# Performance work log

Measured on AMD Instinct MI355X. Metric: run time of the kernel, lower is better.

## Reference

```python
import jax, jax.numpy as jnp
import numpy as np

LORA_RANK = 16
LORA_ALPHA = 16
LORA_SCALE = LORA_ALPHA / LORA_RANK


def setup_inputs() -> dict:
    key = jax.random.key(0)
    k1, k2, k3, k4, k5 = jax.random.split(key, 5)
    B, S, D_IN, D_OUT, N_LORA, R = 8, 2048, 4096, 4096, 3, LORA_RANK
    std = 1.0 / np.sqrt(D_IN)
    x = jax.random.normal(k1, (B, S, D_IN), dtype=jnp.float32)
    weight = jax.random.truncated_normal(k2, -3.0, 3.0, (D_OUT, D_IN), dtype=jnp.float32) * std
    bias = jax.random.normal(k3, (D_OUT,), dtype=jnp.float32) * 0.01
    lora_A = jax.random.normal(k4, (N_LORA, R, D_IN), dtype=jnp.float32) * std
    lora_B = jax.random.normal(k5, (N_LORA, D_OUT, R), dtype=jnp.float32) * 0.02
    # segment starts: samples 0-1 -> no LoRA (index 0 reserved), 2-3 -> adapter 1, 4-5 -> adapter 2, 6-7 -> adapter 3
    lora_start_indices = jnp.arange(4, dtype=jnp.int64) * 2
    return {"x": x, "weight": weight, "bias": bias, "lora_A": lora_A,
            "lora_B": lora_B, "lora_start_indices": lora_start_indices}


def reference(x, weight, bias, lora_A, lora_B, lora_start_indices):
    # Base linear: y = x @ W^T + b   (torch: weight @ x_column)
    y = jnp.einsum('bsd,od->bso', x, weight) + bias  # [B,S,D_out]
    B = x.shape[0]
    # Map each batch sample to its segment (SGMV-style dispatch over contiguous segments).
    seg = jnp.searchsorted(lora_start_indices, jnp.arange(B), side='right') - 1  # [B], 0 = no LoRA
    adapter_idx = jnp.clip(seg - 1, 0, lora_A.shape[0] - 1)
    A = lora_A[adapter_idx]   # [B, r, D_in]  (tiny gather)
    Bw = lora_B[adapter_idx]  # [B, D_out, r]
    lo = jnp.einsum('bsr,bor->bso', jnp.einsum('bsd,brd->bsr', x, A), Bw) * LORA_SCALE
    use_lora = (seg > 0)[:, None, None]
    return y + jnp.where(use_lora, lo, jnp.zeros((), dtype=y.dtype))
```

## Files before the change

### kernel.cpp

```cpp
#include <hip/hip_runtime.h>


typedef __attribute__((ext_vector_type(8))) short short8;
typedef __attribute__((ext_vector_type(4))) float f32x4;
typedef __attribute__((ext_vector_type(4))) unsigned short u16x4;
typedef unsigned short u16;

typedef __attribute__((address_space(1))) void as1_void;
typedef __attribute__((address_space(3))) void as3_void;

#define M_DIM 16384
#define N_DIM 4096
#define K_DIM 4096
#define K2 8192
#define BM 256
#define BN 256
#define BK 64

__device__ __forceinline__ u16 f2bf(float f) {
  union { float f; unsigned u; } v; v.f = f;
  unsigned r = (v.u + 0x7FFFu + ((v.u >> 16) & 1u)) >> 16;
  return (u16)r;
}
__device__ __forceinline__ float bf2f(u16 u) {
  union { unsigned u; float f; } v; v.u = ((unsigned)u) << 16;
  return v.f;
}
__device__ __forceinline__ void gload16(const void* g, void* lds) {
  __builtin_amdgcn_global_load_lds((as1_void*)g, (as3_void*)lds, 16, 0, 0);
}
__device__ __forceinline__ int seg_of_batch(const int* starts, int b) {
  int seg = -1;
#pragma unroll
  for (int i = 0; i < 4; ++i) seg += (starts[i] <= b) ? 1 : 0;
  return seg;
}

#define VMCNT(n) asm volatile("s_waitcnt vmcnt(" #n ")" ::: "memory")

__global__ __launch_bounds__(256) void prep_kernel(
    const float* __restrict__ x, const float* __restrict__ wgt,
    const float* __restrict__ lA, const float* __restrict__ lB,
    u16* __restrict__ xbf, u16* __restrict__ wbf,
    u16* __restrict__ abf, u16* __restrict__ bw) {
  const long long NX4 = 16777216LL;
  const long long NW4 = 4194304LL;
  const long long NA4 = 49152LL;
  const long long NB  = 12288LL;
  const long long total = NX4 + NW4 + NA4 + NB;
  const f32x4* x4 = (const f32x4*)x;
  const f32x4* w4 = (const f32x4*)wgt;
  const f32x4* a4 = (const f32x4*)lA;
  u16x4* xo = (u16x4*)xbf;
  u16x4* wo = (u16x4*)wbf;
  u16x4* ao = (u16x4*)abf;
  for (long long i = (long long)blockIdx.x * blockDim.x + threadIdx.x; i < total;
       i += (long long)gridDim.x * blockDim.x) {
    if (i < NX4) {
      f32x4 v = x4[i];
      u16x4 o = {f2bf(v.x), f2bf(v.y), f2bf(v.z), f2bf(v.w)};
      xo[i] = o;
    } else if (i < NX4 + NW4) {
      long long j = i - NX4;
      f32x4 v = w4[j];
      u16x4 o = {f2bf(v.x), f2bf(v.y), f2bf(v.z), f2bf(v.w)};
      wo[j] = o;
    } else if (i < NX4 + NW4 + NA4) {
      long long j = i - NX4 - NW4;
      f32x4 v = a4[j];
      u16x4 o = {f2bf(v.x), f2bf(v.y), f2bf(v.z), f2bf(v.w)};
      ao[j] = o;
    } else {
      long long p = i - NX4 - NW4 - NA4;
      const float* src = lB + p * 16;
      u16* dst = bw + p * 32;
#pragma unroll
      for (int j = 0; j < 16; ++j) dst[j] = f2bf(src[j]);
#pragma unroll
      for (int j = 16; j < 32; ++j) dst[j] = 0;
    }
  }
}

__global__ __launch_bounds__(256) void ucompute_kernel(
    const u16* __restrict__ xbf, const u16* __restrict__ abf,
    const int* __restrict__ starts, u16* __restrict__ u) {
  const int l = threadIdx.x & 63;
  const int w = threadIdx.x >> 6;
  const int mbase = blockIdx.x * 16 + w * 4;
  const int b = mbase >> 11;
  const int seg = seg_of_batch(starts, b);
  const int use = seg > 0;
  int ad = seg - 1; ad = ad < 0 ? 0 : (ad > 2 ? 2 : ad);

  float acc[4][16];
#pragma unroll
  for (int row = 0; row < 4; ++row)
#pragma unroll
    for (int r = 0; r < 16; ++r) acc[row][r] = 0.f;

  if (use) {
    const u16* xr = xbf + (size_t)mbase * K_DIM + l * 8;
    const u16* ar = abf + (size_t)ad * (16 * K_DIM) + l * 8;
    for (int pass = 0; pass < 8; ++pass) {
      const int off = pass * 512;
      float xv[4][8];
#pragma unroll
      for (int row = 0; row < 4; ++row) {
        short8 xs = *(const short8*)(xr + (size_t)row * K_DIM + off);
#pragma unroll
        for (int j = 0; j < 8; ++j) xv[row][j] = bf2f((u16)xs[j]);
      }
#pragma unroll
      for (int r = 0; r < 16; ++r) {
        short8 av = *(const short8*)(ar + (size_t)r * K_DIM + off);
#pragma unroll
        for (int j = 0; j < 8; ++j) {
          float a = bf2f((u16)av[j]);
#pragma unroll
          for (int row = 0; row < 4; ++row) acc[row][r] += xv[row][j] * a;
        }
      }
    }
  }
#pragma unroll
  for (int row = 0; row < 4; ++row) {
    float myval = 0.f;
#pragma unroll
    for (int r = 0; r < 16; ++r) {
      float v = acc[row][r];
      v += __shfl_xor(v, 32);
      v += __shfl_xor(v, 16);
      v += __shfl_xor(v, 8);
      v += __shfl_xor(v, 4);
      v += __shfl_xor(v, 2);
      v += __shfl_xor(v, 1);
      if (l == r) myval = v;
    }
    if (l < 32) u[(size_t)(mbase + row) * 32 + l] = (l < 16) ? f2bf(myval) : (u16)0;
  }
}


#define STAGE_A(buf, ih, kt) do { \
  gload16(aSrc + (size_t)((ih)*64) * K2 + (size_t)(kt)*128, \
          &As[buf][((ih)*64) * BK] + w * 512); \
  gload16(aSrc + (size_t)((ih)*64 + 128) * K2 + (size_t)(kt)*128, \
          &As[buf][((ih)*64 + 128) * BK] + w * 512); \
} while (0)
#define STAGE_B(buf, jh, kt) do { \
  gload16(bSrc + (size_t)((jh)*32) * K2 + (size_t)(kt)*128, \
          &Bs[buf][((jh)*32 + (w >> 2)*64) * BK] + (w & 3) * 512); \
  gload16(bSrc + (size_t)((jh)*32 + 128) * K2 + (size_t)(kt)*128, \
          &Bs[buf][((jh)*32 + (w >> 2)*64 + 128) * BK] + (w & 3) * 512); \
} while (0)

#define PHASE(buf, ih, jh, STAGE_STMT, WAIT_STMT) do { \
  short8 aF0[4], aF1[4], bF0[2], bF1[2]; \
  _Pragma("unroll") \
  for (int i2 = 0; i2 < 4; ++i2) { \
    const u16* ar = &As[buf][(wr*128 + (ih)*64 + i2*16 + fm) * BK]; \
    aF0[i2] = *(const short8*)(ar + c0); \
    aF1[i2] = *(const short8*)(ar + c1); \
  } \
  _Pragma("unroll") \
  for (int j2 = 0; j2 < 2; ++j2) { \
    const u16* br = &Bs[buf][(wc*64 + (jh)*32 + j2*16 + fm) * BK]; \
    bF0[j2] = *(const short8*)(br + c0); \
    bF1[j2] = *(const short8*)(br + c1); \
  } \
  STAGE_STMT; \
  WAIT_STMT; \
  __builtin_amdgcn_s_barrier(); \
  __builtin_amdgcn_s_setprio(1); \
  _Pragma("unroll") \
  for (int i2 = 0; i2 < 4; ++i2) \
  _Pragma("unroll") \
  for (int j2 = 0; j2 < 2; ++j2) { \
    acc[(ih)*4 + i2][(jh)*2 + j2] = __builtin_amdgcn_mfma_f32_16x16x32_bf16( \
        aF0[i2], bF0[j2], acc[(ih)*4 + i2][(jh)*2 + j2], 0, 0, 0); \
    acc[(ih)*4 + i2][(jh)*2 + j2] = __builtin_amdgcn_mfma_f32_16x16x32_bf16( \
        aF1[i2], bF1[j2], acc[(ih)*4 + i2][(jh)*2 + j2], 0, 0, 0); \
  } \
  __builtin_amdgcn_s_setprio(0); \
  __builtin_amdgcn_s_barrier(); \
} while (0)

__global__ __launch_bounds__(512, 2) void gemm8_kernel(
    const u16* __restrict__ xbf, const u16* __restrict__ wbf,
    const float* __restrict__ bias, const u16* __restrict__ ubuf,
    const u16* __restrict__ bwpad, const int* __restrict__ starts,
    float* __restrict__ out) {
  __shared__ u16 As[2][BM * BK];
  __shared__ u16 Bs[2][BN * BK];

  const int tid = threadIdx.x;
  const int l = tid & 63;
  const int w = tid >> 6;

  const int bid = blockIdx.x;
  const int nb = (bid & 7) * 128 + (bid >> 3);
  const int m0 = (nb >> 4) << 8;
  const int n0 = (nb & 15) << 8;

  const int b = m0 >> 11;
  const int seg = seg_of_batch(starts, b);
  int ad = seg - 1; ad = ad < 0 ? 0 : (ad > 2 ? 2 : ad);

  const int lrow = l >> 3;
  const int swzslot = (l & 7) ^ lrow;
  const char* aSrc = (const char*)xbf +
      (size_t)(m0 + 8 * w + lrow) * K2 + swzslot * 16;
  const char* bSrc = (const char*)wbf +
      (size_t)(n0 + (w >> 2) * 64 + (w & 3) * 8 + lrow) * K2 + swzslot * 16;

  const int fm = l & 15;
  const int q = l >> 4;
  const int wr = w >> 2;
  const int wc = w & 3;
  const int c0 = ((q ^ (fm & 7)) * 8);
  const int c1 = (((q + 4) ^ (fm & 7)) * 8);

  f32x4 acc[8][4];
  const f32x4 z4 = {0.f, 0.f, 0.f, 0.f};
#pragma unroll
  for (int i = 0; i < 8; ++i)
#pragma unroll
    for (int j = 0; j < 4; ++j) acc[i][j] = z4;

  STAGE_A(0, 0, 0); STAGE_B(0, 0, 0); STAGE_A(0, 1, 0); STAGE_B(0, 1, 0);
  STAGE_A(1, 0, 1); STAGE_B(1, 0, 1);
  VMCNT(4);
  __builtin_amdgcn_s_barrier();

  for (int s = 0; s < 32; ++s) {
    const int t1 = 2 * s + 1;
    const int t2 = 2 * s + 2;
    const int t3 = 2 * s + 3;
    const bool more = (s < 31);
    PHASE(0, 0, 0, STAGE_A(1, 1, t1), (void)0);
    PHASE(0, 0, 1, STAGE_B(1, 1, t1), (void)0);
    PHASE(0, 1, 0, if (more) STAGE_A(0, 0, t2), (void)0);
    PHASE(0, 1, 1, if (more) STAGE_B(0, 0, t2),
          if (more) VMCNT(4); else VMCNT(0));
    PHASE(1, 0, 0, if (more) STAGE_A(0, 1, t2), (void)0);
    PHASE(1, 0, 1, if (more) STAGE_B(0, 1, t2), (void)0);
    PHASE(1, 1, 0, if (more) STAGE_A(1, 0, t3), (void)0);
    PHASE(1, 1, 1, if (more) STAGE_B(1, 0, t3),
          if (more) VMCNT(4); else VMCNT(0));
  }

  {
    u16* la = &As[0][0];
    u16* lb = &Bs[0][0];
    const int ls = l & 3;
    const int lr = l >> 2;
    const char* uSrc = (const char*)ubuf +
        (size_t)(m0 + 16 * w + lr) * 64 + ls * 16;
    const char* vSrc = (const char*)bwpad +
        ((size_t)ad * N_DIM + n0 + 16 * w + lr) * 64 + ls * 16;
    gload16(uSrc, la + (16 * w) * 32);
    gload16(uSrc + (size_t)128 * 64, la + (128 + 16 * w) * 32);
    gload16(vSrc, lb + (16 * w) * 32);
    gload16(vSrc + (size_t)128 * 64, lb + (128 + 16 * w) * 32);
    VMCNT(0);
    __builtin_amdgcn_s_barrier();
    short8 aF[8], bF[4];
#pragma unroll
    for (int i = 0; i < 8; ++i)
      aF[i] = *(const short8*)(la + (wr * 128 + i * 16 + fm) * 32 + q * 8);
#pragma unroll
    for (int j = 0; j < 4; ++j)
      bF[j] = *(const short8*)(lb + (wc * 64 + j * 16 + fm) * 32 + q * 8);
#pragma unroll
    for (int i = 0; i < 8; ++i)
#pragma unroll
      for (int j = 0; j < 4; ++j)
        acc[i][j] = __builtin_amdgcn_mfma_f32_16x16x32_bf16(aF[i], bF[j],
                                                            acc[i][j], 0, 0, 0);
  }

  float bv[4];
#pragma unroll
  for (int j = 0; j < 4; ++j) bv[j] = bias[n0 + wc * 64 + j * 16 + fm];
#pragma unroll
  for (int i = 0; i < 8; ++i) {
#pragma unroll
    for (int ii = 0; ii < 4; ++ii) {
      const int m = m0 + wr * 128 + i * 16 + q * 4 + ii;
      float* orow = out + (size_t)m * N_DIM + n0 + wc * 64 + fm;
#pragma unroll
      for (int j = 0; j < 4; ++j) orow[j * 16] = acc[i][j][ii] + bv[j];
    }
  }
}

__global__ __launch_bounds__(256) void u_f32_kernel(
    const float* __restrict__ x, const float* __restrict__ lA,
    const int* __restrict__ starts, float* __restrict__ u) {
  const int l = threadIdx.x & 63;
  const int w = threadIdx.x >> 6;
  const int m = blockIdx.x * 4 + w;
  const int b = m >> 11;
  const int seg = seg_of_batch(starts, b);
  const int use = seg > 0;
  int ad = seg - 1; ad = ad < 0 ? 0 : (ad > 2 ? 2 : ad);
  float acc[16];
#pragma unroll
  for (int r = 0; r < 16; ++r) acc[r] = 0.f;
  if (use) {
    const float* xr = x + (size_t)m * K_DIM + l * 4;
    const float* ar = lA + (size_t)ad * (16 * K_DIM) + l * 4;
    for (int pass = 0; pass < 16; ++pass) {
      const int off = pass * 256;
      f32x4 xv = *(const f32x4*)(xr + off);
#pragma unroll
      for (int r = 0; r < 16; ++r) {
        f32x4 av = *(const f32x4*)(ar + (size_t)r * K_DIM + off);
        acc[r] += xv.x * av.x + xv.y * av.y + xv.z * av.z + xv.w * av.w;
      }
    }
  }
  float myval = 0.f;
#pragma unroll
  for (int r = 0; r < 16; ++r) {
    float v = acc[r];
    v += __shfl_xor(v, 32);
    v += __shfl_xor(v, 16);
    v += __shfl_xor(v, 8);
    v += __shfl_xor(v, 4);
    v += __shfl_xor(v, 2);
    v += __shfl_xor(v, 1);
    if (l == r) myval = v;
  }
  if (l < 16) u[(size_t)m * 16 + l] = myval;
}

__global__ __launch_bounds__(256) void gemm_f32_fallback(
    const float* __restrict__ x, const float* __restrict__ wgt,
    const float* __restrict__ bias, const float* __restrict__ lB,
    const float* __restrict__ u, const int* __restrict__ starts,
    float* __restrict__ out) {
  __shared__ float xs[4096];
  const int m = blockIdx.y;
  const int n0 = blockIdx.x * 256;
  const int t = threadIdx.x;
  const f32x4* xr4 = (const f32x4*)(x + (size_t)m * K_DIM);
  f32x4* xs4 = (f32x4*)xs;
  for (int i = t; i < 1024; i += 256) xs4[i] = xr4[i];
  __syncthreads();
  const int b = m >> 11;
  const int seg = seg_of_batch(starts, b);
  const int use = seg > 0;
  int ad = seg - 1; ad = ad < 0 ? 0 : (ad > 2 ? 2 : ad);
  const int n = n0 + t;
  const f32x4* wr = (const f32x4*)(wgt + (size_t)n * K_DIM);
  float acc = 0.f;
  for (int kk = 0; kk < 1024; ++kk) {
    f32x4 wv = wr[kk];
    f32x4 xv = xs4[kk];
    acc += xv.x * wv.x + xv.y * wv.y + xv.z * wv.z + xv.w * wv.w;
  }
  acc += bias[n];
  if (use) {
    const float* Bn = lB + ((size_t)ad * N_DIM + n) * 16;
    const float* um = u + (size_t)m * 16;
    float lo = 0.f;
#pragma unroll
    for (int r = 0; r < 16; ++r) lo += um[r] * Bn[r];
    acc += lo;
  }
  out[(size_t)m * N_DIM + n] = acc;
}

extern "C" void kernel_launch(void* const* d_in, const int* in_sizes, int n_in,
                              void* d_out, int out_size, void* d_ws, size_t ws_size,
                              hipStream_t stream) {
  const float* x    = (const float*)d_in[0];
  const float* wgt  = (const float*)d_in[1];
  const float* bias = (const float*)d_in[2];
  const float* lA   = (const float*)d_in[3];
  const float* lB   = (const float*)d_in[4];
  const int* starts = (const int*)d_in[5];
  float* out = (float*)d_out;

  const size_t XBF_OFF = 0;
  const size_t WBF_OFF = 134217728;
  const size_t ABF_OFF = 167772160;
  const size_t BW_OFF  = 168165376;
  const size_t U_OFF   = 168951808;
  const size_t WS_NEEDED = 170000384;

  if (ws_size >= WS_NEEDED) {
    u16* xbf = (u16*)((char*)d_ws + XBF_OFF);
    u16* wbf = (u16*)((char*)d_ws + WBF_OFF);
    u16* abf = (u16*)((char*)d_ws + ABF_OFF);
    u16* bw  = (u16*)((char*)d_ws + BW_OFF);
    u16* u   = (u16*)((char*)d_ws + U_OFF);
    prep_kernel<<<8192, 256, 0, stream>>>(x, wgt, lA, lB, xbf, wbf, abf, bw);
    ucompute_kernel<<<1024, 256, 0, stream>>>(xbf, abf, starts, u);
    gemm8_kernel<<<1024, 512, 0, stream>>>(xbf, wbf, bias, u, bw, starts, out);
  } else {
    float* uf = (float*)d_ws;
    u_f32_kernel<<<4096, 256, 0, stream>>>(x, lA, starts, uf);
    gemm_f32_fallback<<<dim3(16, 16384), 256, 0, stream>>>(x, wgt, bias, lB, uf, starts, out);
  }
}
```

Baseline: 1.187 ms.

## Reuse LDS fragments across phases with serpentine quadrant order and deeper prefetch

Changes the eight-phase GEMM loop to visit the four output quadrants in a snake order (00,01,11,10). A/B register fragments stay live across phases, so each phase only re-reads the operand half that changed from LDS. The global-to-LDS staging schedule is reordered to match, with one more load group in flight (vmcnt 6 instead of 4). This cuts LDS read traffic per k-step at the cost of more live VGPRs, which could cause spills or pressure occupancy under the launch bound of 2.

After: 1.132 ms. 4.7% less time.

```diff
diff --git a/kernel.cpp b/kernel.cpp
--- a/kernel.cpp
+++ b/kernel.cpp
@@ -155,19 +155,22 @@
           &Bs[buf][((jh)*32 + (w >> 2)*64 + 128) * BK] + (w & 3) * 512); \
 } while (0)
 
-#define PHASE(buf, ih, jh, STAGE_STMT, WAIT_STMT) do { \
-  short8 aF0[4], aF1[4], bF0[2], bF1[2]; \
-  _Pragma("unroll") \
-  for (int i2 = 0; i2 < 4; ++i2) { \
-    const u16* ar = &As[buf][(wr*128 + (ih)*64 + i2*16 + fm) * BK]; \
-    aF0[i2] = *(const short8*)(ar + c0); \
-    aF1[i2] = *(const short8*)(ar + c1); \
+#define PHASE(buf, ih, jh, LA, LB, BARR, STAGE_STMT, WAIT_STMT) do { \
+  if (LA) { \
+    _Pragma("unroll") \
+    for (int i2 = 0; i2 < 4; ++i2) { \
+      const u16* ar = &As[buf][(wr*128 + (ih)*64 + i2*16 + fm) * BK]; \
+      aFr[i2][0] = *(const short8*)(ar + c0); \
+      aFr[i2][1] = *(const short8*)(ar + c1); \
+    } \
   } \
-  _Pragma("unroll") \
-  for (int j2 = 0; j2 < 2; ++j2) { \
-    const u16* br = &Bs[buf][(wc*64 + (jh)*32 + j2*16 + fm) * BK]; \
-    bF0[j2] = *(const short8*)(br + c0); \
-    bF1[j2] = *(const short8*)(br + c1); \
+  if (LB) { \
+    _Pragma("unroll") \
+    for (int j2 = 0; j2 < 2; ++j2) { \
+      const u16* br = &Bs[buf][(wc*64 + (jh)*32 + j2*16 + fm) * BK]; \
+      BARR[j2][0] = *(const short8*)(br + c0); \
+      BARR[j2][1] = *(const short8*)(br + c1); \
+    } \
   } \
   STAGE_STMT; \
   WAIT_STMT; \
@@ -178,9 +181,9 @@
   _Pragma("unroll") \
   for (int j2 = 0; j2 < 2; ++j2) { \
     acc[(ih)*4 + i2][(jh)*2 + j2] = __builtin_amdgcn_mfma_f32_16x16x32_bf16( \
-        aF0[i2], bF0[j2], acc[(ih)*4 + i2][(jh)*2 + j2], 0, 0, 0); \
+        aFr[i2][0], BARR[j2][0], acc[(ih)*4 + i2][(jh)*2 + j2], 0, 0, 0); \
     acc[(ih)*4 + i2][(jh)*2 + j2] = __builtin_amdgcn_mfma_f32_16x16x32_bf16( \
-        aF1[i2], bF1[j2], acc[(ih)*4 + i2][(jh)*2 + j2], 0, 0, 0); \
+        aFr[i2][1], BARR[j2][1], acc[(ih)*4 + i2][(jh)*2 + j2], 0, 0, 0); \
   } \
   __builtin_amdgcn_s_setprio(0); \
   __builtin_amdgcn_s_barrier(); \
@@ -228,9 +231,13 @@
 #pragma unroll
     for (int j = 0; j < 4; ++j) acc[i][j] = z4;
 
-  STAGE_A(0, 0, 0); STAGE_B(0, 0, 0); STAGE_A(0, 1, 0); STAGE_B(0, 1, 0);
-  STAGE_A(1, 0, 1); STAGE_B(1, 0, 1);
-  VMCNT(4);
+  short8 aFr[4][2];
+  short8 bF0r[2][2];
+  short8 bF1r[2][2];
+
+  STAGE_A(0, 0, 0); STAGE_B(0, 0, 0); STAGE_B(0, 1, 0); STAGE_A(0, 1, 0);
+  STAGE_A(1, 0, 1); STAGE_B(1, 1, 1); STAGE_A(1, 1, 1);
+  VMCNT(6);
   __builtin_amdgcn_s_barrier();
 
   for (int s = 0; s < 32; ++s) {
@@ -238,16 +245,16 @@
     const int t2 = 2 * s + 2;
     const int t3 = 2 * s + 3;
     const bool more = (s < 31);
-    PHASE(0, 0, 0, STAGE_A(1, 1, t1), (void)0);
-    PHASE(0, 0, 1, STAGE_B(1, 1, t1), (void)0);
-    PHASE(0, 1, 0, if (more) STAGE_A(0, 0, t2), (void)0);
-    PHASE(0, 1, 1, if (more) STAGE_B(0, 0, t2),
-          if (more) VMCNT(4); else VMCNT(0));
-    PHASE(1, 0, 0, if (more) STAGE_A(0, 1, t2), (void)0);
-    PHASE(1, 0, 1, if (more) STAGE_B(0, 1, t2), (void)0);
-    PHASE(1, 1, 0, if (more) STAGE_A(1, 0, t3), (void)0);
-    PHASE(1, 1, 1, if (more) STAGE_B(1, 0, t3),
-          if (more) VMCNT(4); else VMCNT(0));
+    PHASE(0, 0, 0, 1, 1, bF0r, STAGE_B(1, 0, t1), (void)0);
+    PHASE(0, 0, 1, 0, 1, bF1r, if (more) STAGE_A(0, 0, t2), (void)0);
+    PHASE(0, 1, 1, 1, 0, bF1r, if (more) STAGE_B(0, 1, t2), (void)0);
+    PHASE(0, 1, 0, 0, 0, bF0r, if (more) STAGE_A(0, 1, t2),
+          if (more) VMCNT(6); else VMCNT(0));
+    PHASE(1, 0, 0, 1, 1, bF0r, if (more) STAGE_B(0, 0, t2), (void)0);
+    PHASE(1, 0, 1, 0, 1, bF1r, if (more) STAGE_A(1, 0, t3), (void)0);
+    PHASE(1, 1, 1, 1, 0, bF1r, if (more) STAGE_B(1, 1, t3), (void)0);
+    PHASE(1, 1, 0, 0, 0, bF0r, if (more) STAGE_A(1, 1, t3),
+          if (more) VMCNT(6); else VMCNT(0));
   }
 
   {
```
